# Performance work log

Measured on AMD Instinct MI355X. Metric: run time of the kernel, lower is better.

## Reference

```python
import jax, jax.numpy as jnp
import numpy as np

B, S, D_IN = 2, 2048, 2048
NUM_HEADS, NUM_KV_GROUPS, HEAD_DIM = 32, 8, 64
GROUP_SIZE = NUM_HEADS // NUM_KV_GROUPS  # 4
D_OUT = NUM_HEADS * HEAD_DIM  # 2048


def setup_inputs() -> dict:
    key = jax.random.key(0)
    k1, k2, k3, k4, k5 = jax.random.split(key, 5)
    scale_in = 1.0 / np.sqrt(D_IN)
    scale_out = 1.0 / np.sqrt(D_OUT)
    return {
        "x": jax.random.normal(k1, (B, S, D_IN), dtype=jnp.float32),
        # Linear weights stored torch-style as (out_features, in_features); y = x @ W.T
        "Wq": jax.random.uniform(k2, (D_OUT, D_IN), minval=-scale_in, maxval=scale_in, dtype=jnp.float32),
        "Wk": jax.random.uniform(k3, (NUM_KV_GROUPS * HEAD_DIM, D_IN), minval=-scale_in, maxval=scale_in, dtype=jnp.float32),
        "Wv": jax.random.uniform(k4, (NUM_KV_GROUPS * HEAD_DIM, D_IN), minval=-scale_in, maxval=scale_in, dtype=jnp.float32),
        "Wo": jax.random.uniform(k5, (D_IN, D_OUT), minval=-scale_out, maxval=scale_out, dtype=jnp.float32),
    }


def reference(x, Wq, Wk, Wv, Wo):
    b, s, _ = x.shape
    # Projections
    q = (x @ Wq.T).reshape(b, s, NUM_KV_GROUPS, GROUP_SIZE, HEAD_DIM)  # [b,s,g,r,d]
    k = (x @ Wk.T).reshape(b, s, NUM_KV_GROUPS, HEAD_DIM)              # [b,s,g,d]
    v = (x @ Wv.T).reshape(b, s, NUM_KV_GROUPS, HEAD_DIM)
    # Scores: broadcast each KV group over its group of query heads
    # (equivalent to repeat_interleave of K/V along head dim)
    scores = jnp.einsum("bqgrd,bkgd->bgrqk", q, k) / np.sqrt(HEAD_DIM).astype(jnp.float32)
    causal = jnp.tril(jnp.ones((s, s), dtype=bool))  # True = keep
    scores = jnp.where(causal, scores, jnp.finfo(scores.dtype).min)
    attn = jax.nn.softmax(scores, axis=-1)  # [b,g,r,q,k]
    ctx = jnp.einsum("bgrqk,bkgd->bqgrd", attn, v).reshape(b, s, D_OUT)
    out = ctx @ Wo.T
    # new_kv_cache (un-expanded keys/values, layout [b, g, s, d])
    keys = k.transpose(0, 2, 1, 3)
    values = v.transpose(0, 2, 1, 3)
    return out, (keys, values)
```

## Files before the change

kernel.cpp:

```cpp
#include <hip/hip_runtime.h>


#define B_   2
#define S_   2048
#define DIN  2048
#define NH   32
#define NKV  8
#define HD   64
#define DOUT 2048
#define NQKV 3072

#define QSCALE 0.18033688f

typedef short bf16x8 __attribute__((ext_vector_type(8)));
typedef short bf16x4 __attribute__((ext_vector_type(4)));
typedef float f32x4  __attribute__((ext_vector_type(4)));

__device__ __forceinline__ unsigned short f2bf(float f) {
  unsigned int u = __float_as_uint(f);
  u += 0x7fff + ((u >> 16) & 1);
  return (unsigned short)(u >> 16);
}

__device__ __forceinline__ f32x4 mfma16(bf16x4 a, bf16x4 b, f32x4 c) {
#if __has_builtin(__builtin_amdgcn_mfma_f32_16x16x16bf16_1k)
  return __builtin_amdgcn_mfma_f32_16x16x16bf16_1k(a, b, c, 0, 0, 0);
#else
  asm volatile("v_mfma_f32_16x16x16_bf16 %0, %1, %2, %0" : "+v"(c) : "v"(a), "v"(b));
  return c;
#endif
}

__device__ __forceinline__ void gld_lds16(const void* gptr, void* lptr) {
  __builtin_amdgcn_global_load_lds(
      (const __attribute__((address_space(1))) unsigned int*)gptr,
      (__attribute__((address_space(3))) unsigned int*)lptr,
      16, 0, 0);
}

#define BAR() __builtin_amdgcn_s_barrier()

#define VMCNT(n)                                        \
  do {                                                  \
    asm volatile("s_waitcnt vmcnt(" #n ")");            \
    __builtin_amdgcn_sched_barrier(0);                  \
  } while (0)

__global__ __launch_bounds__(256) void cvt_all(
    const float* __restrict__ x,  const float* __restrict__ Wq,
    const float* __restrict__ Wk, const float* __restrict__ Wv,
    const float* __restrict__ Wo,
    unsigned short* __restrict__ xbf, unsigned short* __restrict__ wqkv,
    unsigned short* __restrict__ wobf) {
  int i = blockIdx.x * blockDim.x + threadIdx.x;
  const float* src; unsigned short* dst; int off;
  if (i < 2097152)      { src = x;  dst = xbf;                  off = i; }
  else if (i < 3145728) { src = Wq; dst = wqkv;                 off = i - 2097152; }
  else if (i < 3407872) { src = Wk; dst = wqkv + 2048 * 2048;   off = i - 3145728; }
  else if (i < 3670016) { src = Wv; dst = wqkv + 2560 * 2048;   off = i - 3407872; }
  else                  { src = Wo; dst = wobf;                 off = i - 3670016; }
  float4 f = ((const float4*)src)[off];
  ushort4 o;
  o.x = f2bf(f.x); o.y = f2bf(f.y); o.z = f2bf(f.z); o.w = f2bf(f.w);
  ((ushort4*)dst)[off] = o;
}

#define MMA_PHASE(MH, NHH, BF)                                                  \
  do {                                                                          \
    __builtin_amdgcn_s_setprio(1);                                              \
    _Pragma("unroll")                                                           \
    for (int kk = 0; kk < 2; ++kk)                                              \
      _Pragma("unroll")                                                         \
      for (int mr = 0; mr < 4; ++mr)                                            \
        _Pragma("unroll")                                                       \
        for (int nr = 0; nr < NR; ++nr)                                         \
          acc[(MH) * 4 + mr][(NHH) * NR + nr] =                                 \
              __builtin_amdgcn_mfma_f32_16x16x32_bf16(                          \
                  af[mr][kk], BF[nr][kk], acc[(MH) * 4 + mr][(NHH) * NR + nr],  \
                  0, 0, 0);                                                     \
    __builtin_amdgcn_s_setprio(0);                                              \
  } while (0)

template <int MODE, int BN, int NTN>
__global__ __launch_bounds__(512, 2) void gemm8p(
    const unsigned short* __restrict__ A,
    const unsigned short* __restrict__ Bm,
    int K,
    unsigned short* __restrict__ qbf,
    unsigned short* __restrict__ kbf,
    unsigned short* __restrict__ vtbf,
    float* __restrict__ kout,
    float* __restrict__ vout,
    float* __restrict__ cout) {
  constexpr int NR = BN / 128;
  constexpr int BHROW = BN / 2;
  __shared__ unsigned short As[2][256 * 64];
  __shared__ unsigned short Bs[2][BN * 64];

  const int tid  = threadIdx.x;
  const int lane = tid & 63;
  const int wave = tid >> 6;
  const int wm   = wave >> 2;
  const int wn   = wave & 3;
  const int quad = lane >> 4;
  const int r16  = lane & 15;

  const int NT = K / 64;

  const int nwg = gridDim.x;
  const int id  = blockIdx.x;
  const int sid = (id & 7) * (nwg >> 3) + (id >> 3);
  const int by  = sid / NTN;
  const int bx  = sid % NTN;
  const int aRowBase = by * 256;
  const int bColBase = bx * BN;

  f32x4 zero = {0.f, 0.f, 0.f, 0.f};
  f32x4 acc[8][2 * NR];
#pragma unroll
  for (int i = 0; i < 8; ++i)
#pragma unroll
    for (int j = 0; j < 2 * NR; ++j) acc[i][j] = zero;

  auto stageA = [&](int dbuf, int h, int t) {
    const int tt = t < NT ? t : NT - 1;
    const int k0 = tt * 64;
#pragma unroll
    for (int i = 0; i < 2; ++i) {
      const int chunk = (i * 8 + wave) * 64 + lane;
      const int row = chunk >> 3;
      const int slot = chunk & 7;
      const int gc = (slot ^ (row & 7)) * 8;
      gld_lds16(A + (size_t)(aRowBase + h * 128 + row) * K + k0 + gc,
                &As[dbuf][h * 8192 + (i * 8 + wave) * 512]);
    }
  };
  auto stageB = [&](int dbuf, int h, int t) {
    const int tt = t < NT ? t : NT - 1;
    const int k0 = tt * 64;
    if constexpr (BN == 256) {
#pragma unroll
      for (int i = 0; i < 2; ++i) {
        const int chunk = (i * 8 + wave) * 64 + lane;
        const int row = chunk >> 3;
        const int slot = chunk & 7;
        const int gc = (slot ^ (row & 7)) * 8;
        gld_lds16(Bm + (size_t)(bColBase + h * 128 + row) * K + k0 + gc,
                  &Bs[dbuf][h * 8192 + (i * 8 + wave) * 512]);
      }
    } else {
      const int chunk = wave * 64 + lane;
      const int row = chunk >> 3;
      const int slot = chunk & 7;
      const int gc = (slot ^ (row & 7)) * 8;
      gld_lds16(Bm + (size_t)(bColBase + h * 64 + row) * K + k0 + gc,
                &Bs[dbuf][h * 4096 + wave * 512]);
    }
  };

  bf16x8 af[4][2];
  bf16x8 b0[NR][2];
  bf16x8 b1[NR][2];

  auto readA = [&](int sbuf, int mh) {
#pragma unroll
    for (int mr = 0; mr < 4; ++mr)
#pragma unroll
      for (int kk = 0; kk < 2; ++kk) {
        const int row = mh * 128 + wm * 64 + mr * 16 + r16;
        const int slot = (kk * 4 + quad) ^ (r16 & 7);
        af[mr][kk] = *(const bf16x8*)&As[sbuf][row * 64 + slot * 8];
      }
  };
  auto readB = [&](int sbuf, int nh, bf16x8 (&bf)[NR][2]) {
#pragma unroll
    for (int nr = 0; nr < NR; ++nr)
#pragma unroll
      for (int kk = 0; kk < 2; ++kk) {
        const int row = nh * BHROW + wn * (BN / 8) + nr * 16 + r16;
        const int slot = (kk * 4 + quad) ^ (r16 & 7);
        bf[nr][kk] = *(const bf16x8*)&Bs[sbuf][row * 64 + slot * 8];
      }
  };

  stageA(0, 0, 0);
  stageA(0, 1, 0);
  stageB(0, 0, 0);
  stageB(0, 1, 0);
  stageA(1, 0, 1);
  if constexpr (BN == 256) VMCNT(4); else VMCNT(3);
  BAR();

  for (int t = 0; t < NT; ++t) {
    const int buf = t & 1, nbuf = buf ^ 1;

    readA(buf, 0);
    readB(buf, 0, b0);
    stageA(nbuf, 1, t + 1);
    BAR();
    MMA_PHASE(0, 0, b0);
    if constexpr (BN == 256) VMCNT(4); else VMCNT(3);
    BAR();

    readB(buf, 1, b1);
    stageB(nbuf, 0, t + 1);
    BAR();
    MMA_PHASE(0, 1, b1);
    BAR();

    readA(buf, 1);
    stageB(nbuf, 1, t + 1);
    BAR();
    MMA_PHASE(1, 0, b0);
    BAR();

    stageA(buf, 0, t + 2);
    BAR();
    MMA_PHASE(1, 1, b1);
    if constexpr (BN == 256) VMCNT(4); else VMCNT(3);
    BAR();
  }
  VMCNT(0);

#pragma unroll
  for (int mi = 0; mi < 8; ++mi) {
    const int mh = mi >> 2, mr = mi & 3;
#pragma unroll
    for (int ni = 0; ni < 2 * NR; ++ni) {
      const int nh = ni / NR, nr = ni % NR;
      const int rowb = aRowBase + mh * 128 + wm * 64 + mr * 16 + quad * 4;
      const int col  = bColBase +
                       (BN == 256 ? nh * 128 + wn * 32 + nr * 16
                                  : nh * 64 + wn * 16) + r16;
#pragma unroll
      for (int reg = 0; reg < 4; ++reg) {
        const float v = acc[mi][ni][reg];
        const int m = rowb + reg;
        if (MODE == 1) {
          cout[(size_t)m * DOUT + col] = v;
        } else {
          if (col < 2048) {
            qbf[(size_t)m * DOUT + col] = f2bf(v * QSCALE);
          } else if (col < 2560) {
            const int gg = (col - 2048) >> 6, d = col & 63;
            const int b = m >> 11, s = m & 2047;
            const size_t idx = ((size_t)(b * NKV + gg) * S_ + s) * HD + d;
            kbf[idx]  = f2bf(v);
            kout[idx] = v;
          } else {
            const int gg = (col - 2560) >> 6, d = col & 63;
            const int b = m >> 11, s = m & 2047;
            vtbf[((size_t)(b * NKV + gg) * HD + d) * S_ + s]  = f2bf(v);
            vout[((size_t)(b * NKV + gg) * S_ + s) * HD + d] = v;
          }
        }
      }
    }
  }
}

__global__ __launch_bounds__(512, 4) void attn_kernel(
    const unsigned short* __restrict__ Q,
    const unsigned short* __restrict__ Kb,
    const unsigned short* __restrict__ VT,
    unsigned short* __restrict__ ctx) {
  __shared__ unsigned short Kbuf[2][4096];
  __shared__ unsigned short Vbuf[2][4096];

  const int tid  = threadIdx.x;
  const int lane = tid & 63;
  const int wave = tid >> 6;
  const int grp  = wave >> 2;
  const int hw   = wave & 3;
  const int quad = lane >> 4;
  const int r16  = lane & 15;
  const int g    = blockIdx.y;
  const int b    = blockIdx.z;
  const int h    = g * 4 + hw;
  const int pairI = blockIdx.x;
  const int q0     = grp ? pairI * 32 : (63 - pairI) * 32;
  const int nT_own = grp ? pairI / 2 + 1 : (63 - pairI) / 2 + 1;
  const int nTa    = (63 - pairI) / 2 + 1;

  const unsigned short* Kh  = Kb + (size_t)(b * NKV + g) * S_ * HD;
  const unsigned short* VTh = VT + (size_t)(b * NKV + g) * HD * S_;

  const int srow   = lane >> 3;
  const int schunk = (lane & 7) ^ srow;

  bf16x8 aq[2][2];
#pragma unroll
  for (int mt = 0; mt < 2; ++mt)
#pragma unroll
    for (int kk = 0; kk < 2; ++kk)
      aq[mt][kk] = *(const bf16x8*)(Q + (size_t)(b * S_ + q0 + mt * 16 + r16) * DOUT +
                                    h * HD + kk * 32 + quad * 8);

  bf16x4 ones4;
#pragma unroll
  for (int i = 0; i < 4; ++i) ones4[i] = (short)0x3F80;

  f32x4 zero = {0.f, 0.f, 0.f, 0.f};
  f32x4 o[2][4];
  f32x4 l[2];
#pragma unroll
  for (int mt = 0; mt < 2; ++mt) {
    l[mt] = zero;
#pragma unroll
    for (int dt = 0; dt < 4; ++dt) o[mt][dt] = zero;
  }

  auto stage = [&](int buf, int kt) {
    const int kbase = kt * 64;
    gld_lds16(Kh + (size_t)(kbase + wave * 8 + srow) * HD + schunk * 8,
              &Kbuf[buf][wave * 512]);
    gld_lds16(VTh + (size_t)(wave * 8 + srow) * S_ + kbase + schunk * 8,
              &Vbuf[buf][wave * 512]);
  };

  stage(0, 0);
  __syncthreads();

  for (int kt = 0; kt < nTa; ++kt) {
    const int buf = kt & 1;
    if (kt + 1 < nTa) stage(buf ^ 1, kt + 1);

    if (kt < nT_own) {
      bf16x8 bk[4][2];
#pragma unroll
      for (int nt = 0; nt < 4; ++nt)
#pragma unroll
        for (int kk = 0; kk < 2; ++kk) {
          const int seg = nt * 2 + (r16 >> 3), r = r16 & 7;
          const int slot = (kk * 4 + quad) ^ r;
          bk[nt][kk] = *(const bf16x8*)&Kbuf[buf][seg * 512 + r * 64 + slot * 8];
        }

      const bool last = (kt == nT_own - 1);
#pragma unroll
      for (int mt = 0; mt < 2; ++mt) {
        f32x4 st[4];
#pragma unroll
        for (int nt = 0; nt < 4; ++nt) st[nt] = zero;
#pragma unroll
        for (int kk = 0; kk < 2; ++kk)
#pragma unroll
          for (int nt = 0; nt < 4; ++nt)
            st[nt] = __builtin_amdgcn_mfma_f32_16x16x32_bf16(bk[nt][kk], aq[mt][kk], st[nt], 0, 0, 0);

        bf16x4 pf[4];
#pragma unroll
        for (int nt = 0; nt < 4; ++nt) {
#pragma unroll
          for (int r = 0; r < 4; ++r) {
            float s = st[nt][r];
            if (last) {
              const int key = kt * 64 + nt * 16 + quad * 4 + r;
              const int row = q0 + mt * 16 + r16;
              if (key > row) s = -1e38f;
            }
            const float p = __builtin_amdgcn_exp2f(s);
            pf[nt][r] = (short)(__float_as_uint(p) >> 16);
          }
        }
#pragma unroll
        for (int nt = 0; nt < 4; ++nt) l[mt] = mfma16(pf[nt], ones4, l[mt]);
#pragma unroll
        for (int dt = 0; dt < 4; ++dt) {
          const int seg = dt * 2 + (r16 >> 3), r = r16 & 7;
#pragma unroll
          for (int nt = 0; nt < 4; ++nt) {
            const int slot = (nt * 2 + (quad >> 1)) ^ r;
            bf16x4 bv = *(const bf16x4*)&Vbuf[buf][seg * 512 + r * 64 + slot * 8 + (quad & 1) * 4];
            o[mt][dt] = mfma16(pf[nt], bv, o[mt][dt]);
          }
        }
      }
    }

    __syncthreads();
  }

#pragma unroll
  for (int mt = 0; mt < 2; ++mt) {
    f32x4 rl;
#pragma unroll
    for (int r = 0; r < 4; ++r) rl[r] = __builtin_amdgcn_rcpf(l[mt][r]);
#pragma unroll
    for (int dt = 0; dt < 4; ++dt)
#pragma unroll
      for (int r = 0; r < 4; ++r) {
        const int qq = q0 + mt * 16 + quad * 4 + r;
        ctx[(size_t)(b * S_ + qq) * DOUT + h * HD + dt * 16 + r16] =
            f2bf(o[mt][dt][r] * rl[r]);
      }
  }
}

extern "C" void kernel_launch(void* const* d_in, const int* in_sizes, int n_in,
                              void* d_out, int out_size, void* d_ws, size_t ws_size,
                              hipStream_t stream) {
  const float* x  = (const float*)d_in[0];
  const float* Wq = (const float*)d_in[1];
  const float* Wk = (const float*)d_in[2];
  const float* Wv = (const float*)d_in[3];
  const float* Wo = (const float*)d_in[4];

  float* out  = (float*)d_out;
  float* keys = out + (size_t)B_ * S_ * DOUT;
  float* vals = keys + (size_t)B_ * NKV * S_ * HD;

  unsigned short* xbf  = (unsigned short*)d_ws;
  unsigned short* wqkv = xbf  + (size_t)B_ * S_ * DIN;
  unsigned short* wobf = wqkv + (size_t)NQKV * DIN;
  unsigned short* qbf  = wobf + (size_t)DIN * DOUT;
  unsigned short* kbf  = qbf  + (size_t)B_ * S_ * DOUT;
  unsigned short* vtbf = kbf  + (size_t)B_ * NKV * S_ * HD;
  unsigned short* ctx  = vtbf + (size_t)B_ * NKV * S_ * HD;

  cvt_all<<<dim3(4718592 / 256), dim3(256), 0, stream>>>(x, Wq, Wk, Wv, Wo,
                                                         xbf, wqkv, wobf);

  gemm8p<0, 256, 12><<<dim3(192), dim3(512), 0, stream>>>(
      xbf, wqkv, DIN, qbf, kbf, vtbf, keys, vals, nullptr);

  attn_kernel<<<dim3(32, NKV, B_), dim3(512), 0, stream>>>(qbf, kbf, vtbf, ctx);

  gemm8p<1, 128, 16><<<dim3(256), dim3(512), 0, stream>>>(
      ctx, wobf, DOUT, nullptr, nullptr, nullptr, nullptr, nullptr, out);
}
```

Baseline: 318.9 us.

## Unroll GEMM main loop by two and deepen load prefetch pipeline

The GEMM main loop is unrolled by two so buffer indices are compile-time constants. The prologue now issues loads for both stage buffers. B tiles for the next step are prefetched earlier, and the vmcnt waits are relaxed so more global-to-LDS loads stay in flight. Scheduling barriers move out of the wait macro and sit after each barrier. This aims to hide more memory latency behind MFMA phases, at the cost of more code size and possible hazards if NT is odd or the buffer reuse ordering is wrong.

```diff
diff --git a/kernel.cpp b/kernel.cpp
--- a/kernel.cpp
+++ b/kernel.cpp
@@ -39,12 +39,8 @@
 }
 
 #define BAR() __builtin_amdgcn_s_barrier()
-
-#define VMCNT(n)                                        \
-  do {                                                  \
-    asm volatile("s_waitcnt vmcnt(" #n ")");            \
-    __builtin_amdgcn_sched_barrier(0);                  \
-  } while (0)
+#define SB()  __builtin_amdgcn_sched_barrier(0)
+#define VMCNT(n) asm volatile("s_waitcnt vmcnt(" #n ")")
 
 __global__ __launch_bounds__(256) void cvt_all(
     const float* __restrict__ x,  const float* __restrict__ Wq,
@@ -81,6 +77,12 @@
     __builtin_amdgcn_s_setprio(0);                                              \
   } while (0)
 
+#define WAITW()                                   \
+  do {                                            \
+    if constexpr (BN == 256) VMCNT(6);            \
+    else                     VMCNT(4);            \
+  } while (0)
+
 template <int MODE, int BN, int NTN>
 __global__ __launch_bounds__(512, 2) void gemm8p(
     const unsigned short* __restrict__ A,
@@ -184,41 +186,66 @@
   };
 
   stageA(0, 0, 0);
-  stageA(0, 1, 0);
   stageB(0, 0, 0);
   stageB(0, 1, 0);
+  stageA(0, 1, 0);
   stageA(1, 0, 1);
-  if constexpr (BN == 256) VMCNT(4); else VMCNT(3);
-  BAR();
-
-  for (int t = 0; t < NT; ++t) {
-    const int buf = t & 1, nbuf = buf ^ 1;
-
-    readA(buf, 0);
-    readB(buf, 0, b0);
-    stageA(nbuf, 1, t + 1);
+  stageB(1, 0, 1);
+  stageB(1, 1, 1);
+  WAITW();
+  BAR(); SB();
+
+  const int NIT = NT / 2;
+  for (int i = 0; i < NIT; ++i) {
+    const int e2 = 2 * i + 2, o2 = 2 * i + 3;
+
+    readA(0, 0); readB(0, 0, b0);
+    stageA(1, 1, 2 * i + 1);
     BAR();
     MMA_PHASE(0, 0, b0);
-    if constexpr (BN == 256) VMCNT(4); else VMCNT(3);
-    BAR();
-
-    readB(buf, 1, b1);
-    stageB(nbuf, 0, t + 1);
+    BAR(); SB();
+
+    readB(0, 1, b1);
+    stageA(0, 0, e2);
     BAR();
     MMA_PHASE(0, 1, b1);
-    BAR();
-
-    readA(buf, 1);
-    stageB(nbuf, 1, t + 1);
+    BAR(); SB();
+
+    readA(0, 1);
+    stageB(0, 0, e2);
     BAR();
     MMA_PHASE(1, 0, b0);
-    BAR();
-
-    stageA(buf, 0, t + 2);
+    BAR(); SB();
+
+    stageB(0, 1, e2);
     BAR();
     MMA_PHASE(1, 1, b1);
-    if constexpr (BN == 256) VMCNT(4); else VMCNT(3);
-    BAR();
+    WAITW();
+    BAR(); SB();
+
+    readA(1, 0); readB(1, 0, b0);
+    stageA(0, 1, e2);
+    BAR();
+    MMA_PHASE(0, 0, b0);
+    BAR(); SB();
+
+    readB(1, 1, b1);
+    stageA(1, 0, o2);
+    BAR();
+    MMA_PHASE(0, 1, b1);
+    BAR(); SB();
+
+    readA(1, 1);
+    stageB(1, 0, o2);
+    BAR();
+    MMA_PHASE(1, 0, b0);
+    BAR(); SB();
+
+    stageB(1, 1, o2);
+    BAR();
+    MMA_PHASE(1, 1, b1);
+    WAITW();
+    BAR(); SB();
   }
   VMCNT(0);
 
```

New measurement: 310.0 us. -2.8%, faster.
